# Kernel tuning notes

Hardware: AMD Instinct MI355X
Metric: run time of the kernel (lower is better)

Reference implementation:

```python
import jax, jax.numpy as jnp
import numpy as np
from jax import lax


def _gru(x, h, Wih, Whh, bih, bhh):
    # PyTorch GRU cell: gates order (r, z, n)
    gi = x @ Wih.T + bih
    gh = h @ Whh.T + bhh
    ir, iz, inn = jnp.split(gi, 3, axis=-1)
    hr, hz, hn = jnp.split(gh, 3, axis=-1)
    r = jax.nn.sigmoid(ir + hr)
    z = jax.nn.sigmoid(iz + hz)
    n = jnp.tanh(inn + r * hn)
    return (1.0 - z) * n + z * h


def setup_inputs() -> dict:
    key = jax.random.key(0)
    ks = jax.random.split(key, 20)
    B, T, D, H, V, S = 128, 80, 4096, 1024, 6000, 10
    s = 0.02
    inp = {
        "data": jax.random.normal(ks[0], (B, T, D), dtype=jnp.float32),
        "mask": jnp.ones((B, S), dtype=jnp.float32),
        "target": jax.random.randint(ks[1], (B, S), 0, V),
        "sent_len": S,
        "enc_Wih": jax.random.normal(ks[2], (3 * H, D), dtype=jnp.float32) * s,
        "enc_Whh": jax.random.normal(ks[3], (3 * H, H), dtype=jnp.float32) * s,
        "enc_bih": jax.random.normal(ks[4], (3 * H,), dtype=jnp.float32) * s,
        "enc_bhh": jax.random.normal(ks[5], (3 * H,), dtype=jnp.float32) * s,
        "dec_Wih": jax.random.normal(ks[6], (3 * H, H), dtype=jnp.float32) * s,
        "dec_Whh": jax.random.normal(ks[7], (3 * H, H), dtype=jnp.float32) * s,
        "dec_bih": jax.random.normal(ks[8], (3 * H,), dtype=jnp.float32) * s,
        "dec_bhh": jax.random.normal(ks[9], (3 * H,), dtype=jnp.float32) * s,
        "lin1_W": jax.random.normal(ks[10], (H, 2 * H), dtype=jnp.float32) * s,
        "lin1_b": jnp.zeros((H,), dtype=jnp.float32),
        "lin2_W": jax.random.normal(ks[11], (V, H), dtype=jnp.float32) * s,
        "lin2_b": jnp.zeros((V,), dtype=jnp.float32),
        "embed": jax.random.normal(ks[12], (V, H), dtype=jnp.float32) * s,
    }
    return inp


def reference(data, mask, target, sent_len,
              enc_Wih, enc_Whh, enc_bih, enc_bhh,
              dec_Wih, dec_Whh, dec_bih, dec_bhh,
              lin1_W, lin1_b, lin2_W, lin2_b, embed):
    B = data.shape[0]
    H = lin1_b.shape[0]
    W1a = lin1_W[:, :H]   # acts on encoder hidden half
    W1b = lin1_W[:, H:]   # acts on embedded word half

    eh0 = jnp.zeros((B, H), dtype=data.dtype)
    dh0 = jnp.zeros((B, H), dtype=data.dtype)

    # ---- encode phase: feed video features; decoder sees [enc_hid, 0] ----
    def enc_step(carry, x_t):
        eh, dh = carry
        eh = _gru(x_t, eh, enc_Wih, enc_Whh, enc_bih, enc_bhh)
        u = jax.nn.relu(eh @ W1a.T + lin1_b)  # zeros half contributes nothing
        dh = _gru(u, dh, dec_Wih, dec_Whh, dec_bih, dec_bhh)
        return (eh, dh), None

    (eh, dh), _ = lax.scan(enc_step, (eh0, dh0), jnp.swapaxes(data, 0, 1))

    # ---- decode phase: encoder input is zeros; decoder sees [enc_hid, embed(word)] ----
    ir0, iz0, in0 = jnp.split(enc_bih, 3)  # zero-input encoder gates

    def dec_step(carry, tgt_t):
        eh, dh, word = carry
        gh = eh @ enc_Whh.T + enc_bhh
        hr, hz, hn = jnp.split(gh, 3, axis=-1)
        r = jax.nn.sigmoid(ir0 + hr)
        z = jax.nn.sigmoid(iz0 + hz)
        n = jnp.tanh(in0 + r * hn)
        eh = (1.0 - z) * n + z * eh

        emb = embed[word]  # [B, H]
        u = jax.nn.relu(eh @ W1a.T + emb @ W1b.T + lin1_b)
        dh = _gru(u, dh, dec_Wih, dec_Whh, dec_bih, dec_bhh)
        logp = jax.nn.log_softmax(dh @ lin2_W.T + lin2_b, axis=-1)  # [B, V]
        new_word = jnp.argmax(logp, axis=1).astype(jnp.int32)
        loss_t = -jnp.mean(logp[jnp.arange(B), tgt_t])  # NLLLoss (mask unused, as in source)
        return (eh, dh, new_word), (loss_t, new_word[0], new_word[1])

    word0 = jnp.ones((B,), dtype=jnp.int32)
    (_, _, _), (losses, sent, sent2) = lax.scan(dec_step, (eh, dh, word0), jnp.swapaxes(target, 0, 1))
    return jnp.sum(losses), sent, sent2
```

## Files before the change

kernel.cpp:

```cpp
#include <hip/hip_runtime.h>
#include <math.h>
#include <float.h>

#define B_ 128
#define T_ 80
#define D_ 4096
#define H_ 1024
#define V_ 6000
#define S_ 10
#define G3 (3*H_)
#define KSPLIT 4

typedef unsigned short ushort_t;
typedef __attribute__((ext_vector_type(8))) short s16x8;
typedef __attribute__((ext_vector_type(4))) float fx4;

__device__ float    g_gi[(size_t)B_*T_*G3];
__device__ ushort_t g_Ah[(size_t)B_*T_*D_];
__device__ ushort_t g_Al[(size_t)B_*T_*D_];
__device__ ushort_t g_Bh[(size_t)G3*D_];
__device__ ushort_t g_Bl[(size_t)G3*D_];
__device__ ushort_t g_Whh_h[G3*H_],  g_Whh_l[G3*H_];
__device__ ushort_t g_dWih_h[G3*H_], g_dWih_l[G3*H_];
__device__ ushort_t g_dWhh_h[G3*H_], g_dWhh_l[G3*H_];
__device__ ushort_t g_l1h[H_*2*H_],  g_l1l[H_*2*H_];
__device__ float g_ghp [KSPLIT*B_*G3];
__device__ float g_gi2p[KSPLIT*B_*G3];
__device__ float g_gh2p[KSPLIT*B_*G3];
__device__ float g_up  [KSPLIT*B_*H_];
__device__ float g_eh[B_*H_];
__device__ float g_dh[B_*H_];
__device__ ushort_t g_ehh[B_*H_], g_ehl[B_*H_];
__device__ ushort_t g_dhh[B_*H_], g_dhl[B_*H_];
__device__ ushort_t g_uh[B_*H_],  g_ul[B_*H_];
__device__ ushort_t g_cath[B_*2*H_], g_catl[B_*2*H_];
__device__ float g_logits[B_*V_];
__device__ int   g_word[B_];

__device__ inline void split1(float x, ushort_t& hi, ushort_t& lo) {
    unsigned u = __float_as_uint(x);
    unsigned rh = u + 0x7FFF + ((u >> 16) & 1);
    hi = (ushort_t)(rh >> 16);
    float fhi = __uint_as_float((unsigned)hi << 16);
    float d = x - fhi;
    unsigned u2 = __float_as_uint(d);
    unsigned rl = u2 + 0x7FFF + ((u2 >> 16) & 1);
    lo = (ushort_t)(rl >> 16);
}

__global__ __launch_bounds__(256) void split_bf16(
    const float* __restrict__ x, ushort_t* __restrict__ hi,
    ushort_t* __restrict__ lo, int n4)
{
    int i = blockIdx.x * 256 + threadIdx.x;
    if (i >= n4) return;
    float4 v = ((const float4*)x)[i];
    ushort_t h0,h1,h2,h3,l0,l1,l2,l3;
    split1(v.x,h0,l0); split1(v.y,h1,l1); split1(v.z,h2,l2); split1(v.w,h3,l3);
    ushort_t* hp = hi + (size_t)i*4;  hp[0]=h0; hp[1]=h1; hp[2]=h2; hp[3]=h3;
    ushort_t* lp = lo + (size_t)i*4;  lp[0]=l0; lp[1]=l1; lp[2]=l2; lp[3]=l3;
}

__device__ inline void gld16(const ushort_t* g, void* l) {
    __builtin_amdgcn_global_load_lds(
        (const __attribute__((address_space(1))) void*)(const void*)g,
        (__attribute__((address_space(3))) void*)l, 16, 0, 0);
}

__global__ __launch_bounds__(256) void gemm_x3(
    const ushort_t* __restrict__ Ah, const ushort_t* __restrict__ Al, int lda,
    const ushort_t* __restrict__ Bh, const ushort_t* __restrict__ Bl, int ldw,
    const float* __restrict__ bias,
    float* __restrict__ C,
    int M, int N, int K, int kchunks,
    const ushort_t* __restrict__ A2h, const ushort_t* __restrict__ A2l,
    const ushort_t* __restrict__ B2h, const ushort_t* __restrict__ B2l,
    float* __restrict__ C2)
{
    int z = blockIdx.z;
    int kc = z;
    if (z >= kchunks) { kc = z - kchunks; Ah=A2h; Al=A2l; Bh=B2h; Bl=B2l; C=C2; }

    __shared__ ushort_t sAh[2][128*32], sAl[2][128*32];
    __shared__ ushort_t sBh[2][128*32], sBl[2][128*32];

    const int tid  = threadIdx.x;
    const int bm   = blockIdx.y * 128, bn = blockIdx.x * 128;
    const int wave = tid >> 6, lane = tid & 63;
    const int wr   = (wave >> 1) * 64, wc = (wave & 1) * 64;
    const int r    = lane & 15, g = lane >> 4;

    fx4 acc[4][4] = {};

    const int kper = K / kchunks;
    const int kbeg = kc * kper;
    const int nt   = kper / 32;

#define STAGE(buf, k0)                                                        \
    {                                                                         \
      _Pragma("unroll")                                                       \
      for (int i_ = 0; i_ < 2; ++i_) {                                        \
        const int o_   = (tid + i_*256) * 16;    \
        const int row_ = o_ >> 6;                                             \
        const int el_  = (o_ & 63) >> 1;                                      \
        const size_t ga_ = (size_t)(bm + row_) * lda + (k0) + el_;            \
        const size_t gb_ = (size_t)(bn + row_) * ldw + (k0) + el_;            \
        const int lb_ = (wave*64 + i_*256) * 16;   \
        gld16(Ah + ga_, (char*)&sAh[buf][0] + lb_);                           \
        gld16(Al + ga_, (char*)&sAl[buf][0] + lb_);                           \
        gld16(Bh + gb_, (char*)&sBh[buf][0] + lb_);                           \
        gld16(Bl + gb_, (char*)&sBl[buf][0] + lb_);                           \
      }                                                                       \
    }

    int cur = 0;
    STAGE(0, kbeg)
    __syncthreads();

    for (int t = 0; t < nt; ++t) {
        if (t + 1 < nt) STAGE(cur ^ 1, kbeg + (t+1)*32)

        s16x8 a_h[4], a_l[4], b_h[4], b_l[4];
#pragma unroll
        for (int i = 0; i < 4; ++i) {
            const int ao = (wr + i*16 + r)*32 + g*8;
            const int bo = (wc + i*16 + r)*32 + g*8;
            a_h[i] = *(const s16x8*)&sAh[cur][ao];
            a_l[i] = *(const s16x8*)&sAl[cur][ao];
            b_h[i] = *(const s16x8*)&sBh[cur][bo];
            b_l[i] = *(const s16x8*)&sBl[cur][bo];
        }
#pragma unroll
        for (int i = 0; i < 4; ++i)
#pragma unroll
            for (int j = 0; j < 4; ++j) {
                acc[i][j] = __builtin_amdgcn_mfma_f32_16x16x32_bf16(a_h[i], b_h[j], acc[i][j], 0, 0, 0);
                acc[i][j] = __builtin_amdgcn_mfma_f32_16x16x32_bf16(a_l[i], b_h[j], acc[i][j], 0, 0, 0);
                acc[i][j] = __builtin_amdgcn_mfma_f32_16x16x32_bf16(a_h[i], b_l[j], acc[i][j], 0, 0, 0);
            }
        __syncthreads();
        cur ^= 1;
    }
#undef STAGE

    float* Cw = C + (size_t)kc * M * N;
#pragma unroll
    for (int i = 0; i < 4; ++i)
#pragma unroll
        for (int j = 0; j < 4; ++j)
#pragma unroll
            for (int reg = 0; reg < 4; ++reg) {
                const int row = bm + wr + i*16 + g*4 + reg;
                const int col = bn + wc + j*16 + r;
                float v = acc[i][j][reg];
                if (kchunks == 1 && bias) v += bias[col];
                Cw[(size_t)row * N + col] = v;
            }
}

#define BM 64
#define BN 64
#define BK 16

__global__ __launch_bounds__(256) void gemm_wt(
    const float* __restrict__ A, int lda,
    const float* __restrict__ W, int ldw,
    const float* __restrict__ bias,
    float* __restrict__ C, int ldc,
    int M, int N, int K)
{
    __shared__ float As[BK][BM];
    __shared__ float Ws[BK][BN];
    const int tid = threadIdx.x;
    const int bm = blockIdx.y * BM;
    const int bn = blockIdx.x * BN;
    const int lr = tid >> 2;
    const int lc = (tid & 3) << 2;
    const int tr = (tid >> 4) << 2;
    const int tc = (tid & 15) << 2;

    float acc[4][4] = {};
    for (int k0 = 0; k0 < K; k0 += BK) {
        {
            const int gr = bm + lr;
            float4 av = *(const float4*)(A + (size_t)gr * lda + k0 + lc);
            As[lc+0][lr] = av.x; As[lc+1][lr] = av.y;
            As[lc+2][lr] = av.z; As[lc+3][lr] = av.w;
            const int wr2 = bn + lr;
            float4 wv = make_float4(0.f,0.f,0.f,0.f);
            if (wr2 < N) wv = *(const float4*)(W + (size_t)wr2 * ldw + k0 + lc);
            Ws[lc+0][lr] = wv.x; Ws[lc+1][lr] = wv.y;
            Ws[lc+2][lr] = wv.z; Ws[lc+3][lr] = wv.w;
        }
        __syncthreads();
#pragma unroll
        for (int k = 0; k < BK; ++k) {
            float4 a4 = *(const float4*)&As[k][tr];
            float4 b4 = *(const float4*)&Ws[k][tc];
            float ar[4] = {a4.x,a4.y,a4.z,a4.w};
            float br[4] = {b4.x,b4.y,b4.z,b4.w};
#pragma unroll
            for (int i = 0; i < 4; ++i)
#pragma unroll
                for (int j = 0; j < 4; ++j)
                    acc[i][j] = fmaf(ar[i], br[j], acc[i][j]);
        }
        __syncthreads();
    }
#pragma unroll
    for (int i = 0; i < 4; ++i) {
        const int m = bm + tr + i;
#pragma unroll
        for (int j = 0; j < 4; ++j) {
            const int n = bn + tc + j;
            if (n < N) C[(size_t)m * ldc + n] = acc[i][j] + bias[n];
        }
    }
}

__global__ __launch_bounds__(256) void gru_update2(
    const float* __restrict__ GI, int gi_rstride, int gi_nsplit,
    const float* __restrict__ bih,
    const float* __restrict__ GHp, const float* __restrict__ bhh,
    float* __restrict__ h, ushort_t* __restrict__ hh, ushort_t* __restrict__ hl)
{
    const int idx = blockIdx.x * 256 + threadIdx.x;
    const int b = idx >> 10;
    const int j = idx & (H_ - 1);
    float ir, iz, inn;
    if (gi_nsplit == 0) {
        const float* gi = GI + (size_t)b * gi_rstride;
        ir = gi[j]; iz = gi[H_ + j]; inn = gi[2*H_ + j];
    } else {
        ir = bih[j]; iz = bih[H_ + j]; inn = bih[2*H_ + j];
        const float* p = GI + (size_t)b * G3;
#pragma unroll
        for (int s = 0; s < KSPLIT; ++s) {
            ir += p[j]; iz += p[H_ + j]; inn += p[2*H_ + j];
            p += (size_t)B_ * G3;
        }
    }
    float hr = bhh[j], hz = bhh[H_ + j], hn = bhh[2*H_ + j];
    const float* q = GHp + (size_t)b * G3;
#pragma unroll
    for (int s = 0; s < KSPLIT; ++s) {
        hr += q[j]; hz += q[H_ + j]; hn += q[2*H_ + j];
        q += (size_t)B_ * G3;
    }
    const float rg = 1.f / (1.f + expf(-(ir + hr)));
    const float zg = 1.f / (1.f + expf(-(iz + hz)));
    const float ng = tanhf(inn + rg * hn);
    const float v = (1.f - zg) * ng + zg * h[idx];
    h[idx] = v;
    split1(v, hh[idx], hl[idx]);
}

__global__ __launch_bounds__(256) void relu_combine(
    const float* __restrict__ Up, const float* __restrict__ bias,
    ushort_t* __restrict__ uh, ushort_t* __restrict__ ul)
{
    const int idx = blockIdx.x * 256 + threadIdx.x;
    const int j = idx & (H_ - 1);
    float v = bias[j];
#pragma unroll
    for (int s = 0; s < KSPLIT; ++s) v += Up[(size_t)s * B_ * H_ + idx];
    v = fmaxf(v, 0.f);
    split1(v, uh[idx], ul[idx]);
}

__global__ __launch_bounds__(256) void cat_eh_emb(
    const ushort_t* __restrict__ ehh, const ushort_t* __restrict__ ehl,
    const float* __restrict__ embed, const int* __restrict__ word,
    ushort_t* __restrict__ cath, ushort_t* __restrict__ catl)
{
    const int idx = blockIdx.x * 256 + threadIdx.x;
    const int b = idx >> 11;
    const int j = idx & (2*H_ - 1);
    if (j < H_) {
        cath[idx] = ehh[b * H_ + j];
        catl[idx] = ehl[b * H_ + j];
    } else {
        float v = embed[(size_t)word[b] * H_ + (j - H_)];
        split1(v, cath[idx], catl[idx]);
    }
}

__global__ __launch_bounds__(256) void init_state(
    float* __restrict__ eh, float* __restrict__ dh,
    ushort_t* __restrict__ ehh, ushort_t* __restrict__ ehl,
    ushort_t* __restrict__ dhh, ushort_t* __restrict__ dhl,
    int* __restrict__ word, float* __restrict__ out)
{
    const int idx = blockIdx.x * 256 + threadIdx.x;
    if (idx < B_*H_) {
        eh[idx] = 0.f; dh[idx] = 0.f;
        ehh[idx] = 0; ehl[idx] = 0; dhh[idx] = 0; dhl[idx] = 0;
    }
    if (idx < B_)    word[idx] = 1;
    if (idx < 21)    out[idx] = 0.f;
}

__global__ __launch_bounds__(256) void softmax_loss(
    const float* __restrict__ logits, const int* __restrict__ target,
    int s, int* __restrict__ word, float* __restrict__ out)
{
    const int b = blockIdx.x;
    const int t = threadIdx.x;
    const float* row = logits + (size_t)b * V_;
    __shared__ float sv[256];
    __shared__ int   si[256];
    __shared__ float ss[256];

    float best = -FLT_MAX; int bi = 0;
    for (int j = t; j < V_; j += 256) {
        float v = row[j];
        if (v > best) { best = v; bi = j; }
    }
    sv[t] = best; si[t] = bi;
    __syncthreads();
    for (int off = 128; off > 0; off >>= 1) {
        if (t < off) {
            float v2 = sv[t + off]; int i2 = si[t + off];
            if (v2 > sv[t] || (v2 == sv[t] && i2 < si[t])) { sv[t] = v2; si[t] = i2; }
        }
        __syncthreads();
    }
    const float m = sv[0];
    const int amax = si[0];

    float sum = 0.f;
    for (int j = t; j < V_; j += 256) sum += expf(row[j] - m);
    ss[t] = sum;
    __syncthreads();
    for (int off = 128; off > 0; off >>= 1) {
        if (t < off) ss[t] += ss[t + off];
        __syncthreads();
    }
    if (t == 0) {
        const float lse = m + logf(ss[0]);
        const int tgt = target[b * S_ + s];
        const float logp = row[tgt] - lse;
        atomicAdd(&out[0], -logp * (1.0f / (float)B_));
        word[b] = amax;
        if (b == 0) out[1 + s]  = (float)amax;
        if (b == 1) out[11 + s] = (float)amax;
    }
}

static inline void launch_x3(hipStream_t st,
    const ushort_t* Ah, const ushort_t* Al, int lda,
    const ushort_t* Bh, const ushort_t* Bl, int ldw,
    const float* bias, float* C, int M, int N, int K, int kchunks)
{
    dim3 grid(N/128, M/128, kchunks);
    gemm_x3<<<grid, 256, 0, st>>>(Ah, Al, lda, Bh, Bl, ldw, bias, C, M, N, K, kchunks,
                                  nullptr, nullptr, nullptr, nullptr, nullptr);
}

static inline void launch_x3_dual(hipStream_t st,
    const ushort_t* Ah, const ushort_t* Al,
    const ushort_t* Bh, const ushort_t* Bl, float* C,
    const ushort_t* A2h, const ushort_t* A2l,
    const ushort_t* B2h, const ushort_t* B2l, float* C2,
    int M, int N, int K, int kchunks)
{
    dim3 grid(N/128, M/128, 2*kchunks);
    gemm_x3<<<grid, 256, 0, st>>>(Ah, Al, H_, Bh, Bl, H_, nullptr, C, M, N, K, kchunks,
                                  A2h, A2l, B2h, B2l, C2);
}

extern "C" void kernel_launch(void* const* d_in, const int* in_sizes, int n_in,
                              void* d_out, int out_size, void* d_ws, size_t ws_size,
                              hipStream_t stream)
{
    const float* data    = (const float*)d_in[0];
    const int*   target  = (const int*)  d_in[2];
    const float* enc_Wih = (const float*)d_in[4];
    const float* enc_Whh = (const float*)d_in[5];
    const float* enc_bih = (const float*)d_in[6];
    const float* enc_bhh = (const float*)d_in[7];
    const float* dec_Wih = (const float*)d_in[8];
    const float* dec_Whh = (const float*)d_in[9];
    const float* dec_bih = (const float*)d_in[10];
    const float* dec_bhh = (const float*)d_in[11];
    const float* lin1_W  = (const float*)d_in[12];
    const float* lin1_b  = (const float*)d_in[13];
    const float* lin2_W  = (const float*)d_in[14];
    const float* lin2_b  = (const float*)d_in[15];
    const float* embed   = (const float*)d_in[16];
    float* out = (float*)d_out;

    float *gi, *eh, *dh, *logits, *ghp, *gi2p, *gh2p, *up;
    ushort_t *Ah, *Al, *Bh, *Bl, *Whh_h, *Whh_l, *dWih_h, *dWih_l, *dWhh_h, *dWhh_l;
    ushort_t *l1h, *l1l, *ehh, *ehl, *dhh, *dhl, *uh, *ul, *cath, *catl;
    int* word;
    hipGetSymbolAddress((void**)&gi,     HIP_SYMBOL(g_gi));
    hipGetSymbolAddress((void**)&Ah,     HIP_SYMBOL(g_Ah));
    hipGetSymbolAddress((void**)&Al,     HIP_SYMBOL(g_Al));
    hipGetSymbolAddress((void**)&Bh,     HIP_SYMBOL(g_Bh));
    hipGetSymbolAddress((void**)&Bl,     HIP_SYMBOL(g_Bl));
    hipGetSymbolAddress((void**)&Whh_h,  HIP_SYMBOL(g_Whh_h));
    hipGetSymbolAddress((void**)&Whh_l,  HIP_SYMBOL(g_Whh_l));
    hipGetSymbolAddress((void**)&dWih_h, HIP_SYMBOL(g_dWih_h));
    hipGetSymbolAddress((void**)&dWih_l, HIP_SYMBOL(g_dWih_l));
    hipGetSymbolAddress((void**)&dWhh_h, HIP_SYMBOL(g_dWhh_h));
    hipGetSymbolAddress((void**)&dWhh_l, HIP_SYMBOL(g_dWhh_l));
    hipGetSymbolAddress((void**)&l1h,    HIP_SYMBOL(g_l1h));
    hipGetSymbolAddress((void**)&l1l,    HIP_SYMBOL(g_l1l));
    hipGetSymbolAddress((void**)&ghp,    HIP_SYMBOL(g_ghp));
    hipGetSymbolAddress((void**)&gi2p,   HIP_SYMBOL(g_gi2p));
    hipGetSymbolAddress((void**)&gh2p,   HIP_SYMBOL(g_gh2p));
    hipGetSymbolAddress((void**)&up,     HIP_SYMBOL(g_up));
    hipGetSymbolAddress((void**)&eh,     HIP_SYMBOL(g_eh));
    hipGetSymbolAddress((void**)&dh,     HIP_SYMBOL(g_dh));
    hipGetSymbolAddress((void**)&ehh,    HIP_SYMBOL(g_ehh));
    hipGetSymbolAddress((void**)&ehl,    HIP_SYMBOL(g_ehl));
    hipGetSymbolAddress((void**)&dhh,    HIP_SYMBOL(g_dhh));
    hipGetSymbolAddress((void**)&dhl,    HIP_SYMBOL(g_dhl));
    hipGetSymbolAddress((void**)&uh,     HIP_SYMBOL(g_uh));
    hipGetSymbolAddress((void**)&ul,     HIP_SYMBOL(g_ul));
    hipGetSymbolAddress((void**)&cath,   HIP_SYMBOL(g_cath));
    hipGetSymbolAddress((void**)&catl,   HIP_SYMBOL(g_catl));
    hipGetSymbolAddress((void**)&logits, HIP_SYMBOL(g_logits));
    hipGetSymbolAddress((void**)&word,   HIP_SYMBOL(g_word));

    init_state<<<512, 256, 0, stream>>>(eh, dh, ehh, ehl, dhh, dhl, word, out);

    split_bf16<<<(B_*T_*D_/4 + 255)/256, 256, 0, stream>>>(data,    Ah, Al, B_*T_*D_/4);
    split_bf16<<<(G3*D_/4   + 255)/256, 256, 0, stream>>>(enc_Wih, Bh, Bl, G3*D_/4);
    split_bf16<<<(G3*H_/4   + 255)/256, 256, 0, stream>>>(enc_Whh, Whh_h, Whh_l, G3*H_/4);
    split_bf16<<<(G3*H_/4   + 255)/256, 256, 0, stream>>>(dec_Wih, dWih_h, dWih_l, G3*H_/4);
    split_bf16<<<(G3*H_/4   + 255)/256, 256, 0, stream>>>(dec_Whh, dWhh_h, dWhh_l, G3*H_/4);
    split_bf16<<<(H_*2*H_/4 + 255)/256, 256, 0, stream>>>(lin1_W,  l1h, l1l, H_*2*H_/4);

    launch_x3(stream, Ah, Al, D_, Bh, Bl, D_, enc_bih, gi, B_*T_, G3, D_, 1);

    for (int t = 0; t < T_; ++t) {
        launch_x3(stream, ehh, ehl, H_, Whh_h, Whh_l, H_, nullptr, ghp, B_, G3, H_, KSPLIT);
        gru_update2<<<512, 256, 0, stream>>>(gi + (size_t)t * G3, T_ * G3, 0, nullptr,
                                             ghp, enc_bhh, eh, ehh, ehl);
        launch_x3(stream, ehh, ehl, H_, l1h, l1l, 2*H_, nullptr, up, B_, H_, H_, KSPLIT);
        relu_combine<<<512, 256, 0, stream>>>(up, lin1_b, uh, ul);
        launch_x3_dual(stream, uh, ul, dWih_h, dWih_l, gi2p,
                               dhh, dhl, dWhh_h, dWhh_l, gh2p, B_, G3, H_, KSPLIT);
        gru_update2<<<512, 256, 0, stream>>>(gi2p, 0, KSPLIT, dec_bih,
                                             gh2p, dec_bhh, dh, dhh, dhl);
    }

    for (int s = 0; s < S_; ++s) {
        launch_x3(stream, ehh, ehl, H_, Whh_h, Whh_l, H_, nullptr, ghp, B_, G3, H_, KSPLIT);
        gru_update2<<<512, 256, 0, stream>>>(enc_bih, 0, 0, nullptr,
                                             ghp, enc_bhh, eh, ehh, ehl);
        cat_eh_emb<<<1024, 256, 0, stream>>>(ehh, ehl, embed, word, cath, catl);
        launch_x3(stream, cath, catl, 2*H_, l1h, l1l, 2*H_, nullptr, up, B_, H_, 2*H_, KSPLIT);
        relu_combine<<<512, 256, 0, stream>>>(up, lin1_b, uh, ul);
        launch_x3_dual(stream, uh, ul, dWih_h, dWih_l, gi2p,
                               dhh, dhl, dWhh_h, dWhh_l, gh2p, B_, G3, H_, KSPLIT);
        gru_update2<<<512, 256, 0, stream>>>(gi2p, 0, KSPLIT, dec_bih,
                                             gh2p, dec_bhh, dh, dhh, dhl);
        { dim3 grid((V_+BN-1)/BN, B_/BM, 1);
          gemm_wt<<<grid, 256, 0, stream>>>(dh, H_, lin2_W, H_, lin2_b, logits, V_, B_, V_, H_); }
        softmax_loss<<<B_, 256, 0, stream>>>(logits, target, s, word, out);
    }
}
```

Measured before the change: 7.508 ms.

## Fuse encode-phase recurrence into persistent kernel with grid barriers; MFMA vocab GEMM

Replaces the per-timestep chain of six kernel launches in the encode phase with a single persistent 256-block kernel that runs GEMM jobs and GRU/ReLU elementwise updates, separated by software grid barriers. The decoder GRU update is deferred and overlapped with the next step's encoder update. The output vocab projection also switches from a scalar fp32 GEMM to the split-bf16 MFMA GEMM with two K-chunks, and the partials are summed inside softmax. The intent is to cut launch overhead and serialization across 80 steps, at the cost of requiring all blocks to be co-resident and relying on atomic spin barriers.

```diff
diff --git a/kernel.cpp b/kernel.cpp
--- a/kernel.cpp
+++ b/kernel.cpp
@@ -7,9 +7,11 @@
 #define D_ 4096
 #define H_ 1024
 #define V_ 6000
+#define VP 6016
 #define S_ 10
 #define G3 (3*H_)
 #define KSPLIT 4
+#define NBLK 256
 
 typedef unsigned short ushort_t;
 typedef __attribute__((ext_vector_type(8))) short s16x8;
@@ -24,6 +26,7 @@
 __device__ ushort_t g_dWih_h[G3*H_], g_dWih_l[G3*H_];
 __device__ ushort_t g_dWhh_h[G3*H_], g_dWhh_l[G3*H_];
 __device__ ushort_t g_l1h[H_*2*H_],  g_l1l[H_*2*H_];
+__device__ ushort_t g_l2h[(size_t)VP*H_], g_l2l[(size_t)VP*H_];
 __device__ float g_ghp [KSPLIT*B_*G3];
 __device__ float g_gi2p[KSPLIT*B_*G3];
 __device__ float g_gh2p[KSPLIT*B_*G3];
@@ -34,10 +37,11 @@
 __device__ ushort_t g_dhh[B_*H_], g_dhl[B_*H_];
 __device__ ushort_t g_uh[B_*H_],  g_ul[B_*H_];
 __device__ ushort_t g_cath[B_*2*H_], g_catl[B_*2*H_];
-__device__ float g_logits[B_*V_];
+__device__ float g_logitsp[2*B_*VP];
 __device__ int   g_word[B_];
-
-__device__ inline void split1(float x, ushort_t& hi, ushort_t& lo) {
+__device__ int   g_bar[32];
+
+__device__ __forceinline__ void split1(float x, ushort_t& hi, ushort_t& lo) {
     unsigned u = __float_as_uint(x);
     unsigned rh = u + 0x7FFF + ((u >> 16) & 1);
     hi = (ushort_t)(rh >> 16);
@@ -61,10 +65,18 @@
     ushort_t* lp = lo + (size_t)i*4;  lp[0]=l0; lp[1]=l1; lp[2]=l2; lp[3]=l3;
 }
 
-__device__ inline void gld16(const ushort_t* g, void* l) {
+__device__ __forceinline__ void gld16(const ushort_t* g, void* l) {
     __builtin_amdgcn_global_load_lds(
         (const __attribute__((address_space(1))) void*)(const void*)g,
         (__attribute__((address_space(3))) void*)l, 16, 0, 0);
+}
+
+__device__ __forceinline__ float gru_elem(float ir,float iz,float inn,
+                                          float hr,float hz,float hn,float hprev){
+    const float r = 1.f/(1.f+expf(-(ir+hr)));
+    const float z = 1.f/(1.f+expf(-(iz+hz)));
+    const float n = tanhf(inn + r*hn);
+    return (1.f-z)*n + z*hprev;
 }
 
 __global__ __launch_bounds__(256) void gemm_x3(
@@ -100,12 +112,12 @@
     {                                                                         \
       _Pragma("unroll")                                                       \
       for (int i_ = 0; i_ < 2; ++i_) {                                        \
-        const int o_   = (tid + i_*256) * 16;    \
+        const int o_   = (tid + i_*256) * 16;                                 \
         const int row_ = o_ >> 6;                                             \
         const int el_  = (o_ & 63) >> 1;                                      \
         const size_t ga_ = (size_t)(bm + row_) * lda + (k0) + el_;            \
         const size_t gb_ = (size_t)(bn + row_) * ldw + (k0) + el_;            \
-        const int lb_ = (wave*64 + i_*256) * 16;   \
+        const int lb_ = (wave*64 + i_*256) * 16;                              \
         gld16(Ah + ga_, (char*)&sAh[buf][0] + lb_);                           \
         gld16(Al + ga_, (char*)&sAl[buf][0] + lb_);                           \
         gld16(Bh + gb_, (char*)&sBh[buf][0] + lb_);                           \
@@ -158,63 +170,228 @@
             }
 }
 
-#define BM 64
-#define BN 64
-#define BK 16
-
-__global__ __launch_bounds__(256) void gemm_wt(
-    const float* __restrict__ A, int lda,
-    const float* __restrict__ W, int ldw,
-    const float* __restrict__ bias,
-    float* __restrict__ C, int ldc,
-    int M, int N, int K)
-{
-    __shared__ float As[BK][BM];
-    __shared__ float Ws[BK][BN];
+struct SmemT {
+    ushort_t Ah[2][128*32];
+    ushort_t Al[2][128*32];
+    ushort_t Bh[2][128*32];
+    ushort_t Bl[2][128*32];
+};
+
+__device__ __forceinline__ void job_x3(SmemT* sm,
+    const ushort_t* __restrict__ Agh, const ushort_t* __restrict__ Agl, int lda,
+    const ushort_t* __restrict__ Wbh, const ushort_t* __restrict__ Wbl, int ldw,
+    int kbeg, int nt,
+    float* __restrict__ Cw, int ldc, int colbase)
+{
+    const int tid  = threadIdx.x;
+    const int wave = tid >> 6, lane = tid & 63;
+    const int wr   = (wave >> 1) * 64, wc = (wave & 1) * 64;
+    const int r    = lane & 15, g = lane >> 4;
+    fx4 acc[4][4] = {};
+
+#define JSTAGE(buf, k0)                                                       \
+    {                                                                         \
+      _Pragma("unroll")                                                       \
+      for (int i_ = 0; i_ < 2; ++i_) {                                        \
+        const int o_   = (tid + i_*256) * 16;                                 \
+        const int row_ = o_ >> 6;                                             \
+        const int el_  = (o_ & 63) >> 1;                                      \
+        const size_t ga_ = (size_t)row_ * lda + (k0) + el_;                   \
+        const size_t gb_ = (size_t)row_ * ldw + (k0) + el_;                   \
+        const int lb_ = (wave*64 + i_*256) * 16;                              \
+        gld16(Agh + ga_, (char*)&sm->Ah[buf][0] + lb_);                       \
+        gld16(Agl + ga_, (char*)&sm->Al[buf][0] + lb_);                       \
+        gld16(Wbh + gb_, (char*)&sm->Bh[buf][0] + lb_);                       \
+        gld16(Wbl + gb_, (char*)&sm->Bl[buf][0] + lb_);                       \
+      }                                                                       \
+    }
+
+    int cur = 0;
+    JSTAGE(0, kbeg)
+    __syncthreads();
+    for (int t = 0; t < nt; ++t) {
+        if (t + 1 < nt) JSTAGE(cur ^ 1, kbeg + (t+1)*32)
+        s16x8 a_h[4], a_l[4], b_h[4], b_l[4];
+#pragma unroll
+        for (int i = 0; i < 4; ++i) {
+            const int ao = (wr + i*16 + r)*32 + g*8;
+            const int bo = (wc + i*16 + r)*32 + g*8;
+            a_h[i] = *(const s16x8*)&sm->Ah[cur][ao];
+            a_l[i] = *(const s16x8*)&sm->Al[cur][ao];
+            b_h[i] = *(const s16x8*)&sm->Bh[cur][bo];
+            b_l[i] = *(const s16x8*)&sm->Bl[cur][bo];
+        }
+#pragma unroll
+        for (int i = 0; i < 4; ++i)
+#pragma unroll
+            for (int j = 0; j < 4; ++j) {
+                acc[i][j] = __builtin_amdgcn_mfma_f32_16x16x32_bf16(a_h[i], b_h[j], acc[i][j], 0, 0, 0);
+                acc[i][j] = __builtin_amdgcn_mfma_f32_16x16x32_bf16(a_l[i], b_h[j], acc[i][j], 0, 0, 0);
+                acc[i][j] = __builtin_amdgcn_mfma_f32_16x16x32_bf16(a_h[i], b_l[j], acc[i][j], 0, 0, 0);
+            }
+        __syncthreads();
+        cur ^= 1;
+    }
+#undef JSTAGE
+
+#pragma unroll
+    for (int i = 0; i < 4; ++i)
+#pragma unroll
+        for (int j = 0; j < 4; ++j)
+#pragma unroll
+            for (int reg = 0; reg < 4; ++reg)
+                Cw[(size_t)(wr + i*16 + g*4 + reg) * ldc + colbase + wc + j*16 + r]
+                    = acc[i][j][reg];
+}
+
+__device__ __forceinline__ void gbar(int* cnt, int* gen, int* lg) {
+    __syncthreads();
+    if (threadIdx.x == 0) {
+        __threadfence();
+        const int g = *lg;
+        const int prev = __hip_atomic_fetch_add(cnt, 1, __ATOMIC_ACQ_REL,
+                                                __HIP_MEMORY_SCOPE_AGENT);
+        if (prev == NBLK - 1) {
+            __hip_atomic_store(cnt, 0, __ATOMIC_RELAXED, __HIP_MEMORY_SCOPE_AGENT);
+            __hip_atomic_store(gen, g + 1, __ATOMIC_RELEASE, __HIP_MEMORY_SCOPE_AGENT);
+        } else {
+            while (__hip_atomic_load(gen, __ATOMIC_ACQUIRE,
+                                     __HIP_MEMORY_SCOPE_AGENT) == g)
+                __builtin_amdgcn_s_sleep(4);
+        }
+        __threadfence();
+        *lg = g + 1;
+    }
+    __syncthreads();
+}
+
+__device__ __forceinline__ void dec_update(int idx,
+    const float* __restrict__ gi2p, const float* __restrict__ gh2p,
+    const float* __restrict__ dec_bih, const float* __restrict__ dec_bhh,
+    float* __restrict__ dh, ushort_t* __restrict__ dhh, ushort_t* __restrict__ dhl)
+{
+    const int b = idx >> 10, j = idx & (H_ - 1);
+    float ir = dec_bih[j], iz = dec_bih[H_+j], inn = dec_bih[2*H_+j];
+    const float* p = gi2p + (size_t)b * G3;
+#pragma unroll
+    for (int s2 = 0; s2 < KSPLIT; ++s2) {
+        ir += p[j]; iz += p[H_+j]; inn += p[2*H_+j];
+        p += (size_t)B_ * G3;
+    }
+    float hr = dec_bhh[j], hz = dec_bhh[H_+j], hn = dec_bhh[2*H_+j];
+    const float* q = gh2p + (size_t)b * G3;
+#pragma unroll
+    for (int s2 = 0; s2 < KSPLIT; ++s2) {
+        hr += q[j]; hz += q[H_+j]; hn += q[2*H_+j];
+        q += (size_t)B_ * G3;
+    }
+    const float v = gru_elem(ir, iz, inn, hr, hz, hn, dh[idx]);
+    dh[idx] = v;
+    split1(v, dhh[idx], dhl[idx]);
+}
+
+__global__ __launch_bounds__(256) void enc_persist(
+    const float* __restrict__ gi,
+    const ushort_t* __restrict__ Whh_h, const ushort_t* __restrict__ Whh_l,
+    const ushort_t* __restrict__ l1h,   const ushort_t* __restrict__ l1l,
+    const ushort_t* __restrict__ dWih_h,const ushort_t* __restrict__ dWih_l,
+    const ushort_t* __restrict__ dWhh_h,const ushort_t* __restrict__ dWhh_l,
+    const float* __restrict__ enc_bhh,  const float* __restrict__ lin1_b,
+    const float* __restrict__ dec_bih,  const float* __restrict__ dec_bhh,
+    float* __restrict__ eh, ushort_t* __restrict__ ehh, ushort_t* __restrict__ ehl,
+    float* __restrict__ dh, ushort_t* __restrict__ dhh, ushort_t* __restrict__ dhl,
+    ushort_t* __restrict__ uh, ushort_t* __restrict__ ul,
+    float* __restrict__ ghp, float* __restrict__ up,
+    float* __restrict__ gi2p, float* __restrict__ gh2p,
+    int* __restrict__ bar)
+{
+    __shared__ SmemT sm;
+    const int bid = blockIdx.x;
     const int tid = threadIdx.x;
-    const int bm = blockIdx.y * BM;
-    const int bn = blockIdx.x * BN;
-    const int lr = tid >> 2;
-    const int lc = (tid & 3) << 2;
-    const int tr = (tid >> 4) << 2;
-    const int tc = (tid & 15) << 2;
-
-    float acc[4][4] = {};
-    for (int k0 = 0; k0 < K; k0 += BK) {
+    int* cnt = &bar[0];
+    int* gen = &bar[16];
+    int lg = 0;
+
+    for (int t = 0; t < T_; ++t) {
+#pragma unroll
+        for (int rep = 0; rep < 2; ++rep) {
+            const int idx = bid * 512 + rep * 256 + tid;
+            const int b = idx >> 10, j = idx & (H_ - 1);
+            const float* girow = gi + ((size_t)(b * T_ + t)) * G3;
+            float ir = girow[j], iz = girow[H_+j], inn = girow[2*H_+j];
+            float hr = enc_bhh[j], hz = enc_bhh[H_+j], hn = enc_bhh[2*H_+j];
+            const float* q = ghp + (size_t)b * G3;
+#pragma unroll
+            for (int s2 = 0; s2 < KSPLIT; ++s2) {
+                hr += q[j]; hz += q[H_+j]; hn += q[2*H_+j];
+                q += (size_t)B_ * G3;
+            }
+            const float v = gru_elem(ir, iz, inn, hr, hz, hn, eh[idx]);
+            eh[idx] = v;
+            split1(v, ehh[idx], ehl[idx]);
+            if (t > 0)
+                dec_update(idx, gi2p, gh2p, dec_bih, dec_bhh, dh, dhh, dhl);
+        }
+        gbar(cnt, gen, &lg);
+
         {
-            const int gr = bm + lr;
-            float4 av = *(const float4*)(A + (size_t)gr * lda + k0 + lc);
-            As[lc+0][lr] = av.x; As[lc+1][lr] = av.y;
-            As[lc+2][lr] = av.z; As[lc+3][lr] = av.w;
-            const int wr2 = bn + lr;
-            float4 wv = make_float4(0.f,0.f,0.f,0.f);
-            if (wr2 < N) wv = *(const float4*)(W + (size_t)wr2 * ldw + k0 + lc);
-            Ws[lc+0][lr] = wv.x; Ws[lc+1][lr] = wv.y;
-            Ws[lc+2][lr] = wv.z; Ws[lc+3][lr] = wv.w;
-        }
-        __syncthreads();
-#pragma unroll
-        for (int k = 0; k < BK; ++k) {
-            float4 a4 = *(const float4*)&As[k][tr];
-            float4 b4 = *(const float4*)&Ws[k][tc];
-            float ar[4] = {a4.x,a4.y,a4.z,a4.w};
-            float br[4] = {b4.x,b4.y,b4.z,b4.w};
-#pragma unroll
-            for (int i = 0; i < 4; ++i)
-#pragma unroll
-                for (int j = 0; j < 4; ++j)
-                    acc[i][j] = fmaf(ar[i], br[j], acc[i][j]);
-        }
-        __syncthreads();
-    }
-#pragma unroll
-    for (int i = 0; i < 4; ++i) {
-        const int m = bm + tr + i;
-#pragma unroll
-        for (int j = 0; j < 4; ++j) {
-            const int n = bn + tc + j;
-            if (n < N) C[(size_t)m * ldc + n] = acc[i][j] + bias[n];
-        }
+            const ushort_t *jA = nullptr, *jAl2 = nullptr, *jWh = nullptr, *jWl = nullptr;
+            int jldw = H_, jkbeg = 0, jldc = G3, jcol = 0;
+            float* jC = nullptr;
+            if (bid < 96) {
+                const int ntile = bid >> 2, kc = bid & 3;
+                jA = ehh; jAl2 = ehl;
+                jWh = Whh_h + (size_t)ntile * 128 * H_;
+                jWl = Whh_l + (size_t)ntile * 128 * H_;
+                jkbeg = kc * 256; jC = ghp + (size_t)kc * B_ * G3;
+                jldc = G3; jcol = ntile * 128;
+            } else if (bid < 128) {
+                const int jj = bid - 96, ntile = jj >> 2, kc = jj & 3;
+                jA = ehh; jAl2 = ehl;
+                jWh = l1h + (size_t)ntile * 128 * (2*H_);
+                jWl = l1l + (size_t)ntile * 128 * (2*H_);
+                jldw = 2*H_;
+                jkbeg = kc * 256; jC = up + (size_t)kc * B_ * H_;
+                jldc = H_; jcol = ntile * 128;
+            } else if (bid < 224) {
+                const int jj = bid - 128, ntile = jj >> 2, kc = jj & 3;
+                jA = dhh; jAl2 = dhl;
+                jWh = dWhh_h + (size_t)ntile * 128 * H_;
+                jWl = dWhh_l + (size_t)ntile * 128 * H_;
+                jkbeg = kc * 256; jC = gh2p + (size_t)kc * B_ * G3;
+                jldc = G3; jcol = ntile * 128;
+            }
+            if (jA) job_x3(&sm, jA, jAl2, H_, jWh, jWl, jldw, jkbeg, 8, jC, jldc, jcol);
+        }
+        gbar(cnt, gen, &lg);
+
+#pragma unroll
+        for (int rep = 0; rep < 2; ++rep) {
+            const int idx = bid * 512 + rep * 256 + tid;
+            const int j = idx & (H_ - 1);
+            float v = lin1_b[j];
+#pragma unroll
+            for (int s2 = 0; s2 < KSPLIT; ++s2) v += up[(size_t)s2 * B_ * H_ + idx];
+            v = fmaxf(v, 0.f);
+            split1(v, uh[idx], ul[idx]);
+        }
+        gbar(cnt, gen, &lg);
+
+        if (bid < 96) {
+            const int ntile = bid >> 2, kc = bid & 3;
+            job_x3(&sm, uh, ul, H_,
+                   dWih_h + (size_t)ntile * 128 * H_,
+                   dWih_l + (size_t)ntile * 128 * H_, H_,
+                   kc * 256, 8,
+                   gi2p + (size_t)kc * B_ * G3, G3, ntile * 128);
+        }
+        gbar(cnt, gen, &lg);
+    }
+
+#pragma unroll
+    for (int rep = 0; rep < 2; ++rep) {
+        const int idx = bid * 512 + rep * 256 + tid;
+        dec_update(idx, gi2p, gh2p, dec_bih, dec_bhh, dh, dhh, dhl);
     }
 }
 
@@ -247,10 +424,7 @@
         hr += q[j]; hz += q[H_ + j]; hn += q[2*H_ + j];
         q += (size_t)B_ * G3;
     }
-    const float rg = 1.f / (1.f + expf(-(ir + hr)));
-    const float zg = 1.f / (1.f + expf(-(iz + hz)));
-    const float ng = tanhf(inn + rg * hn);
-    const float v = (1.f - zg) * ng + zg * h[idx];
+    const float v = gru_elem(ir, iz, inn, hr, hz, hn, h[idx]);
     h[idx] = v;
     split1(v, hh[idx], hl[idx]);
 }
@@ -289,31 +463,36 @@
     float* __restrict__ eh, float* __restrict__ dh,
     ushort_t* __restrict__ ehh, ushort_t* __restrict__ ehl,
     ushort_t* __restrict__ dhh, ushort_t* __restrict__ dhl,
-    int* __restrict__ word, float* __restrict__ out)
+    int* __restrict__ word, float* __restrict__ out,
+    float* __restrict__ ghp, int* __restrict__ bar)
 {
     const int idx = blockIdx.x * 256 + threadIdx.x;
+    if (idx < KSPLIT*B_*G3) ghp[idx] = 0.f;
     if (idx < B_*H_) {
         eh[idx] = 0.f; dh[idx] = 0.f;
         ehh[idx] = 0; ehl[idx] = 0; dhh[idx] = 0; dhl[idx] = 0;
     }
-    if (idx < B_)    word[idx] = 1;
-    if (idx < 21)    out[idx] = 0.f;
+    if (idx < B_)  word[idx] = 1;
+    if (idx < 21)  out[idx] = 0.f;
+    if (idx < 32)  bar[idx] = 0;
 }
 
 __global__ __launch_bounds__(256) void softmax_loss(
-    const float* __restrict__ logits, const int* __restrict__ target,
-    int s, int* __restrict__ word, float* __restrict__ out)
+    const float* __restrict__ logp, const float* __restrict__ l2b,
+    const int* __restrict__ target, int s, int* __restrict__ word,
+    float* __restrict__ out)
 {
     const int b = blockIdx.x;
     const int t = threadIdx.x;
-    const float* row = logits + (size_t)b * V_;
+    const float* p0 = logp + (size_t)b * VP;
+    const float* p1 = p0 + (size_t)B_ * VP;
     __shared__ float sv[256];
     __shared__ int   si[256];
     __shared__ float ss[256];
 
     float best = -FLT_MAX; int bi = 0;
     for (int j = t; j < V_; j += 256) {
-        float v = row[j];
+        float v = p0[j] + p1[j] + l2b[j];
         if (v > best) { best = v; bi = j; }
     }
     sv[t] = best; si[t] = bi;
@@ -329,7 +508,7 @@
     const int amax = si[0];
 
     float sum = 0.f;
-    for (int j = t; j < V_; j += 256) sum += expf(row[j] - m);
+    for (int j = t; j < V_; j += 256) sum += expf(p0[j] + p1[j] + l2b[j] - m);
     ss[t] = sum;
     __syncthreads();
     for (int off = 128; off > 0; off >>= 1) {
@@ -339,8 +518,8 @@
     if (t == 0) {
         const float lse = m + logf(ss[0]);
         const int tgt = target[b * S_ + s];
-        const float logp = row[tgt] - lse;
-        atomicAdd(&out[0], -logp * (1.0f / (float)B_));
+        const float logit_t = p0[tgt] + p1[tgt] + l2b[tgt];
+        atomicAdd(&out[0], -(logit_t - lse) * (1.0f / (float)B_));
         word[b] = amax;
         if (b == 0) out[1 + s]  = (float)amax;
         if (b == 1) out[11 + s] = (float)amax;
@@ -390,10 +569,10 @@
     const float* embed   = (const float*)d_in[16];
     float* out = (float*)d_out;
 
-    float *gi, *eh, *dh, *logits, *ghp, *gi2p, *gh2p, *up;
+    float *gi, *eh, *dh, *logitsp, *ghp, *gi2p, *gh2p, *up;
     ushort_t *Ah, *Al, *Bh, *Bl, *Whh_h, *Whh_l, *dWih_h, *dWih_l, *dWhh_h, *dWhh_l;
-    ushort_t *l1h, *l1l, *ehh, *ehl, *dhh, *dhl, *uh, *ul, *cath, *catl;
-    int* word;
+    ushort_t *l1h, *l1l, *l2h, *l2l, *ehh, *ehl, *dhh, *dhl, *uh, *ul, *cath, *catl;
+    int *word, *bar;
     hipGetSymbolAddress((void**)&gi,     HIP_SYMBOL(g_gi));
     hipGetSymbolAddress((void**)&Ah,     HIP_SYMBOL(g_Ah));
     hipGetSymbolAddress((void**)&Al,     HIP_SYMBOL(g_Al));
@@ -407,6 +586,8 @@
     hipGetSymbolAddress((void**)&dWhh_l, HIP_SYMBOL(g_dWhh_l));
     hipGetSymbolAddress((void**)&l1h,    HIP_SYMBOL(g_l1h));
     hipGetSymbolAddress((void**)&l1l,    HIP_SYMBOL(g_l1l));
+    hipGetSymbolAddress((void**)&l2h,    HIP_SYMBOL(g_l2h));
+    hipGetSymbolAddress((void**)&l2l,    HIP_SYMBOL(g_l2l));
     hipGetSymbolAddress((void**)&ghp,    HIP_SYMBOL(g_ghp));
     hipGetSymbolAddress((void**)&gi2p,   HIP_SYMBOL(g_gi2p));
     hipGetSymbolAddress((void**)&gh2p,   HIP_SYMBOL(g_gh2p));
@@ -421,10 +602,11 @@
     hipGetSymbolAddress((void**)&ul,     HIP_SYMBOL(g_ul));
     hipGetSymbolAddress((void**)&cath,   HIP_SYMBOL(g_cath));
     hipGetSymbolAddress((void**)&catl,   HIP_SYMBOL(g_catl));
-    hipGetSymbolAddress((void**)&logits, HIP_SYMBOL(g_logits));
+    hipGetSymbolAddress((void**)&logitsp,HIP_SYMBOL(g_logitsp));
     hipGetSymbolAddress((void**)&word,   HIP_SYMBOL(g_word));
-
-    init_state<<<512, 256, 0, stream>>>(eh, dh, ehh, ehl, dhh, dhl, word, out);
+    hipGetSymbolAddress((void**)&bar,    HIP_SYMBOL(g_bar));
+
+    init_state<<<6144, 256, 0, stream>>>(eh, dh, ehh, ehl, dhh, dhl, word, out, ghp, bar);
 
     split_bf16<<<(B_*T_*D_/4 + 255)/256, 256, 0, stream>>>(data,    Ah, Al, B_*T_*D_/4);
     split_bf16<<<(G3*D_/4   + 255)/256, 256, 0, stream>>>(enc_Wih, Bh, Bl, G3*D_/4);
@@ -432,20 +614,15 @@
     split_bf16<<<(G3*H_/4   + 255)/256, 256, 0, stream>>>(dec_Wih, dWih_h, dWih_l, G3*H_/4);
     split_bf16<<<(G3*H_/4   + 255)/256, 256, 0, stream>>>(dec_Whh, dWhh_h, dWhh_l, G3*H_/4);
     split_bf16<<<(H_*2*H_/4 + 255)/256, 256, 0, stream>>>(lin1_W,  l1h, l1l, H_*2*H_/4);
+    split_bf16<<<(V_*H_/4   + 255)/256, 256, 0, stream>>>(lin2_W,  l2h, l2l, V_*H_/4);
 
     launch_x3(stream, Ah, Al, D_, Bh, Bl, D_, enc_bih, gi, B_*T_, G3, D_, 1);
 
-    for (int t = 0; t < T_; ++t) {
-        launch_x3(stream, ehh, ehl, H_, Whh_h, Whh_l, H_, nullptr, ghp, B_, G3, H_, KSPLIT);
-        gru_update2<<<512, 256, 0, stream>>>(gi + (size_t)t * G3, T_ * G3, 0, nullptr,
-                                             ghp, enc_bhh, eh, ehh, ehl);
-        launch_x3(stream, ehh, ehl, H_, l1h, l1l, 2*H_, nullptr, up, B_, H_, H_, KSPLIT);
-        relu_combine<<<512, 256, 0, stream>>>(up, lin1_b, uh, ul);
-        launch_x3_dual(stream, uh, ul, dWih_h, dWih_l, gi2p,
-                               dhh, dhl, dWhh_h, dWhh_l, gh2p, B_, G3, H_, KSPLIT);
-        gru_update2<<<512, 256, 0, stream>>>(gi2p, 0, KSPLIT, dec_bih,
-                                             gh2p, dec_bhh, dh, dhh, dhl);
-    }
+    enc_persist<<<NBLK, 256, 0, stream>>>(
+        gi, Whh_h, Whh_l, l1h, l1l, dWih_h, dWih_l, dWhh_h, dWhh_l,
+        enc_bhh, lin1_b, dec_bih, dec_bhh,
+        eh, ehh, ehl, dh, dhh, dhl, uh, ul,
+        ghp, up, gi2p, gh2p, bar);
 
     for (int s = 0; s < S_; ++s) {
         launch_x3(stream, ehh, ehl, H_, Whh_h, Whh_l, H_, nullptr, ghp, B_, G3, H_, KSPLIT);
@@ -458,8 +635,7 @@
                                dhh, dhl, dWhh_h, dWhh_l, gh2p, B_, G3, H_, KSPLIT);
         gru_update2<<<512, 256, 0, stream>>>(gi2p, 0, KSPLIT, dec_bih,
                                              gh2p, dec_bhh, dh, dhh, dhl);
-        { dim3 grid((V_+BN-1)/BN, B_/BM, 1);
-          gemm_wt<<<grid, 256, 0, stream>>>(dh, H_, lin2_W, H_, lin2_b, logits, V_, B_, V_, H_); }
-        softmax_loss<<<B_, 256, 0, stream>>>(logits, target, s, word, out);
-    }
-}
+        launch_x3(stream, dhh, dhl, H_, l2h, l2l, H_, nullptr, logitsp, B_, VP, H_, 2);
+        softmax_loss<<<B_, 256, 0, stream>>>(logitsp, lin2_b, target, s, word, out);
+    }
+}
```

Result: slower. 24.60 ms (+227.6%).
